# Kernel optimization log

Measured on AMD Instinct MI355X. Metric: run time of the kernel, lower is better.

The kernel has to match this reference:

```python
import jax, jax.numpy as jnp
import numpy as np

W, QN, H, HKV, D, HID = 2, 64, 28, 4, 128, 3584
FRAG_LENS = (8192, 4096, 2048)
THETA = 1e6


def rotate_half(x):
    x1, x2 = jnp.split(x, 2, axis=-1)
    return jnp.concatenate((-x2, x1), axis=-1)


def setup_inputs() -> dict:
    key = jax.random.key(0)
    ks = jax.random.split(key, 16)
    inp = {}
    inp['hidden_states'] = jax.random.normal(ks[0], (W, QN, HID), jnp.float32)
    inp['wq'] = 0.02 * jax.random.normal(ks[1], (H * D, HID), jnp.float32)
    inp['bq'] = 0.02 * jax.random.normal(ks[2], (H * D,), jnp.float32)
    inp['wo'] = 0.02 * jax.random.normal(ks[3], (HID, H * D), jnp.float32)
    for f, L in enumerate(FRAG_LENS):
        inp[f'keys{f}'] = jax.random.normal(ks[4 + f], (HKV, L, D), jnp.float32)
        inp[f'values{f}'] = jax.random.normal(ks[8 + f], (HKV, L, D), jnp.float32)
    # per-fragment query locations: frags 0,1 fully visible; frag 2 causal tail
    loc0 = jnp.full((W, QN), FRAG_LENS[0] - 1, jnp.int32)
    loc1 = jnp.full((W, QN), FRAG_LENS[1] - 1, jnp.int32)
    loc2 = jnp.broadcast_to(FRAG_LENS[2] - QN + jnp.arange(QN, dtype=jnp.int32), (W, QN))
    locations = jnp.stack([loc0, loc1, loc2], axis=0)  # [F, W, QN]
    inp['locations'] = locations
    # RoPE tables per fragment (HF half-rotation convention, base=1e6)
    inv_freq = 1.0 / (THETA ** (jnp.arange(0, D, 2, dtype=jnp.float32) / D))  # [D/2]
    ang = locations.astype(jnp.float32)[..., None] * inv_freq  # [F, W, QN, D/2]
    inp['cos'] = jnp.concatenate([jnp.cos(ang), jnp.cos(ang)], axis=-1)
    inp['sin'] = jnp.concatenate([jnp.sin(ang), jnp.sin(ang)], axis=-1)
    return inp


def _hogwild_attention(q, keys, values, cos, sin, locations, scale):
    # q: [W,H,QN,D]; keys[f]/values[f]: [HKV,L_f,D]; cos/sin: [F,W,QN,D]; locations: [F,W,QN]
    G = q.shape[1] // keys[0].shape[0]  # GQA group size
    logits = []
    for f in range(len(keys)):
        # fragment-specific RoPE on queries
        rq = q * cos[f][:, None] + rotate_half(q) * sin[f][:, None]  # [W,H,QN,D]
        kr = jnp.repeat(keys[f], G, axis=0)  # [H,L,D]
        att = jnp.einsum('whqd,hkd->whqk', rq.astype(jnp.float32), kr.astype(jnp.float32))
        kp = jnp.arange(keys[f].shape[1], dtype=jnp.int32)
        mask = kp[None, None, None, :] > locations[f][:, None, :, None]
        logits.append(jnp.where(mask, -jnp.inf, att))
    qk = jnp.concatenate(logits, axis=-1)  # [W,H,QN,Ktot]
    vals = jnp.concatenate([jnp.repeat(v, G, axis=0) for v in values], axis=1).astype(jnp.float32)
    p = jax.nn.softmax(scale * qk, axis=-1)
    return jnp.einsum('whqk,hkd->whqd', p, vals)  # [W,H,QN,D]


def reference(hidden_states, wq, bq, wo, keys0, keys1, keys2, values0, values1, values2, cos, sin, locations):
    scale = D ** -0.5
    q = hidden_states @ wq.T + bq  # [W,QN,H*D]
    q = q.reshape(W, QN, H, D).transpose(0, 2, 1, 3)  # [W,H,QN,D]
    out = _hogwild_attention(q, [keys0, keys1, keys2], [values0, values1, values2], cos, sin, locations, scale)
    out = out.astype(hidden_states.dtype).transpose(0, 2, 1, 3).reshape(W, QN, H * D)
    return out @ wo.T  # [W,QN,HID]
```

## Files before the change

### kernel.cpp

```cpp
#include <hip/hip_runtime.h>
#include <math.h>


typedef _Float16 f16;
typedef _Float16 h2 __attribute__((ext_vector_type(2)));
typedef _Float16 h4 __attribute__((ext_vector_type(4)));
typedef _Float16 h8 __attribute__((ext_vector_type(8)));
typedef float f32x16 __attribute__((ext_vector_type(16)));

static __device__ __forceinline__ float4 ld4(const float* p){ return *reinterpret_cast<const float4*>(p); }
static __device__ __forceinline__ void st4(float* p, const float4 v){ *reinterpret_cast<float4*>(p) = v; }
static __device__ __forceinline__ h2 pk(float a, float b){
  return __builtin_bit_cast(h2, __builtin_amdgcn_cvt_pkrtz(a, b));
}
static __device__ __forceinline__ h2 sw32(h2 v){
  int i = __builtin_bit_cast(int, v);
  i = __shfl_xor(i, 32, 64);
  return __builtin_bit_cast(h2, i);
}
static __device__ __forceinline__ h8 mk8(h2 a, h2 b, h2 c, h2 d){
  h8 r; r[0]=a[0]; r[1]=a[1]; r[2]=b[0]; r[3]=b[1]; r[4]=c[0]; r[5]=c[1]; r[6]=d[0]; r[7]=d[1]; return r;
}
static __device__ __forceinline__ h4 mk4(h2 a, h2 b){
  h4 r; r[0]=a[0]; r[1]=a[1]; r[2]=b[0]; r[3]=b[1]; return r;
}
static __device__ __forceinline__ h8 ld8h(const f16* p){
  const h4 a = *(const h4*)p;
  const h4 b = *(const h4*)(p + 4);
  h8 r; r[0]=a[0]; r[1]=a[1]; r[2]=a[2]; r[3]=a[3]; r[4]=b[0]; r[5]=b[1]; r[6]=b[2]; r[7]=b[3];
  return r;
}

#define SCALE 0.08838834764831845f

__global__ __launch_bounds__(256) void gemm_mfma_kernel(
    const float* __restrict__ A, const float* __restrict__ Bw,
    const float* __restrict__ bias, float* __restrict__ out, const int qlayout,
    float* __restrict__ Gpart, const int KS)
{
  __shared__ __align__(16) f16 Ah[128][68];
  __shared__ __align__(16) f16 Al[128][68];
  __shared__ __align__(16) f16 Bh[64][68];
  __shared__ __align__(16) f16 Bl[64][68];

  const int t = threadIdx.x;
  const int lane = t & 63;
  const int wv = t >> 6;
  const int l31 = lane & 31;
  const int hh = lane >> 5;
  const int nblk = blockIdx.x * 64;
  const int ks = blockIdx.y;
  const int kspan = 3584 / KS;
  const int kbeg = ks * kspan;

  f32x16 acc0, acc1;
#pragma unroll
  for (int g = 0; g < 16; ++g) { acc0[g] = 0.f; acc1[g] = 0.f; }

  for (int kc = kbeg; kc < kbeg + kspan; kc += 64) {
#pragma unroll
    for (int r = 0; r < 4; ++r) {
      const int li = r * 256 + t;
      const int m = li >> 3;
      const int k8 = (li & 7) * 8;
      const float* p = A + (size_t)m * 3584 + kc + k8;
      const float4 x0 = ld4(p), x1 = ld4(p + 4);
      const h2 a01 = pk(x0.x, x0.y), a23 = pk(x0.z, x0.w);
      const h2 a45 = pk(x1.x, x1.y), a67 = pk(x1.z, x1.w);
      const h2 r01 = pk(x0.x - (float)a01[0], x0.y - (float)a01[1]);
      const h2 r23 = pk(x0.z - (float)a23[0], x0.w - (float)a23[1]);
      const h2 r45 = pk(x1.x - (float)a45[0], x1.y - (float)a45[1]);
      const h2 r67 = pk(x1.z - (float)a67[0], x1.w - (float)a67[1]);
      *(h4*)&Ah[m][k8]     = mk4(a01, a23);
      *(h4*)&Ah[m][k8 + 4] = mk4(a45, a67);
      *(h4*)&Al[m][k8]     = mk4(r01, r23);
      *(h4*)&Al[m][k8 + 4] = mk4(r45, r67);
    }
#pragma unroll
    for (int r = 0; r < 2; ++r) {
      const int li = r * 256 + t;
      const int n = li >> 3;
      const int k8 = (li & 7) * 8;
      const float* p = Bw + (size_t)(nblk + n) * 3584 + kc + k8;
      const float4 x0 = ld4(p), x1 = ld4(p + 4);
      const h2 a01 = pk(x0.x, x0.y), a23 = pk(x0.z, x0.w);
      const h2 a45 = pk(x1.x, x1.y), a67 = pk(x1.z, x1.w);
      const h2 r01 = pk(x0.x - (float)a01[0], x0.y - (float)a01[1]);
      const h2 r23 = pk(x0.z - (float)a23[0], x0.w - (float)a23[1]);
      const h2 r45 = pk(x1.x - (float)a45[0], x1.y - (float)a45[1]);
      const h2 r67 = pk(x1.z - (float)a67[0], x1.w - (float)a67[1]);
      *(h4*)&Bh[n][k8]     = mk4(a01, a23);
      *(h4*)&Bh[n][k8 + 4] = mk4(a45, a67);
      *(h4*)&Bl[n][k8]     = mk4(r01, r23);
      *(h4*)&Bl[n][k8 + 4] = mk4(r45, r67);
    }
    __syncthreads();

#pragma unroll 2
    for (int k16 = 0; k16 < 4; ++k16) {
      const int ko = k16 * 16 + hh * 8;
      const h8 ah  = ld8h(&Ah[wv * 32 + l31][ko]);
      const h8 al  = ld8h(&Al[wv * 32 + l31][ko]);
      const h8 bh0 = ld8h(&Bh[l31][ko]);
      const h8 bl0 = ld8h(&Bl[l31][ko]);
      const h8 bh1 = ld8h(&Bh[32 + l31][ko]);
      const h8 bl1 = ld8h(&Bl[32 + l31][ko]);
      acc0 = __builtin_amdgcn_mfma_f32_32x32x16_f16(ah, bh0, acc0, 0, 0, 0);
      acc0 = __builtin_amdgcn_mfma_f32_32x32x16_f16(ah, bl0, acc0, 0, 0, 0);
      acc0 = __builtin_amdgcn_mfma_f32_32x32x16_f16(al, bh0, acc0, 0, 0, 0);
      acc1 = __builtin_amdgcn_mfma_f32_32x32x16_f16(ah, bh1, acc1, 0, 0, 0);
      acc1 = __builtin_amdgcn_mfma_f32_32x32x16_f16(ah, bl1, acc1, 0, 0, 0);
      acc1 = __builtin_amdgcn_mfma_f32_32x32x16_f16(al, bh1, acc1, 0, 0, 0);
    }
    __syncthreads();
  }

  if (Gpart) {
    float* gp = Gpart + (size_t)ks * 458752;
#pragma unroll
    for (int reg = 0; reg < 16; ++reg) {
      const int m = wv * 32 + (reg & 3) + 8 * (reg >> 2) + 4 * hh;
      gp[(size_t)m * 3584 + nblk + l31]      = acc0[reg];
      gp[(size_t)m * 3584 + nblk + 32 + l31] = acc1[reg];
    }
    return;
  }
#pragma unroll
  for (int reg = 0; reg < 16; ++reg) {
    const int m = wv * 32 + (reg & 3) + 8 * (reg >> 2) + 4 * hh;
#pragma unroll
    for (int nt = 0; nt < 2; ++nt) {
      const int n = nblk + nt * 32 + l31;
      float v = (nt ? acc1[reg] : acc0[reg]) + (bias ? bias[n] : 0.f);
      if (qlayout) {
        const int w = m >> 6, qn = m & 63, hcol = n >> 7, d = n & 127;
        out[(((size_t)(w * 28 + hcol)) * 64 + qn) * 128 + d] = v;
      } else {
        out[(size_t)m * 3584 + n] = v;
      }
    }
  }
}

__global__ __launch_bounds__(256) void gemm_reduce_kernel(
    const float* __restrict__ Gpart, const float* __restrict__ bias,
    float* __restrict__ out, const int KS, const int qlayout)
{
  const int idx = blockIdx.x * 256 + threadIdx.x;
  const int m = idx / 896;
  const int n = (idx - m * 896) * 4;
  float4 a = ld4(Gpart + (size_t)m * 3584 + n);
  for (int ss = 1; ss < KS; ++ss) {
    const float4 b = ld4(Gpart + (size_t)ss * 458752 + (size_t)m * 3584 + n);
    a.x += b.x; a.y += b.y; a.z += b.z; a.w += b.w;
  }
  if (bias) { a.x += bias[n]; a.y += bias[n + 1]; a.z += bias[n + 2]; a.w += bias[n + 3]; }
  if (qlayout) {
    const int w = m >> 6, qn = m & 63, hh = n >> 7, d = n & 127;
    st4(out + (((size_t)(w * 28 + hh)) * 64 + qn) * 128 + d, a);
  } else {
    st4(out + (size_t)m * 3584 + n, a);
  }
}

__global__ __launch_bounds__(256) void vtrans_kernel(
    const float* __restrict__ V0, const float* __restrict__ V1, const float* __restrict__ V2,
    f16* __restrict__ Vt)
{
  __shared__ __align__(16) f16 T[64 * 136];
  const int bid = blockIdx.x;
  const int kvh = bid / 224;
  const int g0 = (bid % 224) * 64;
  const int t = threadIdx.x;
#pragma unroll
  for (int rep = 0; rep < 8; ++rep) {
    const int li = rep * 256 + t;
    const int k = li >> 5;
    const int d0 = (li & 31) * 4;
    const int g = g0 + k;
    const float* src;
    if (g < 8192)       src = V0 + ((size_t)kvh * 8192 + g) * 128 + d0;
    else if (g < 12288) src = V1 + ((size_t)kvh * 4096 + (g - 8192)) * 128 + d0;
    else                src = V2 + ((size_t)kvh * 2048 + (g - 12288)) * 128 + d0;
    const float4 v = ld4(src);
    h2 x = pk(v.x, v.y), y = pk(v.z, v.w);
    h4 q4; q4[0] = x[0]; q4[1] = x[1]; q4[2] = y[0]; q4[3] = y[1];
    *(h4*)((char*)T + k * 272 + d0 * 2) = q4;
  }
  __syncthreads();
#pragma unroll
  for (int rep = 0; rep < 4; ++rep) {
    const int li = rep * 256 + t;
    const int d = li >> 3;
    const int kc = (li & 7) * 8;
    h8 o;
#pragma unroll
    for (int j = 0; j < 8; ++j) o[j] = T[(kc + j) * 136 + d];
    *(h8*)(Vt + ((size_t)kvh * 128 + d) * 14336 + g0 + kc) = o;
  }
}

__global__ __launch_bounds__(512, 4) void attn_mfma_kernel(
    const float* __restrict__ q_ws,
    const float* __restrict__ cosT, const float* __restrict__ sinT,
    const float* __restrict__ K0, const float* __restrict__ K1, const float* __restrict__ K2,
    const float* __restrict__ V0, const float* __restrict__ V1, const float* __restrict__ V2,
    const int* __restrict__ loc,
    const f16* __restrict__ Vt, const int vt16,
    float* __restrict__ attn,
    float* __restrict__ Opart, float* __restrict__ Ml, const int NS)
{
  union ShmU {
    struct { f16 k[128 * 128]; f16 vt[128 * 128]; } t;
    struct { float o[2][32 * 132]; float m[8][32]; float l[8][32];
             float lg[2][32]; float mg[2][32]; } e;
  };
  __shared__ __align__(16) ShmU S;
  __shared__ __align__(16) f16 RQ[64 * 128];

  int unit, s, h, w, kvh;
  if (NS > 1) {
    const int C = 4 * NS;
    const int combo = blockIdx.x % C;
    const int idx = blockIdx.x / C;
    kvh = combo / NS; s = combo % NS;
    const int hh7 = idx % 7;
    w = idx / 7;
    h = kvh * 7 + hh7;
    unit = w * 28 + h;
  } else {
    unit = blockIdx.x; s = 0;
    h = unit % 28; w = unit / 28; kvh = h / 7;
  }

  const int tiles_per = 112 / NS;
  const int tile0 = s * tiles_per;
  const int tile1 = tile0 + tiles_per;

  const int t = threadIdx.x;
  const int lane = t & 63;
  const int wv = t >> 6;
  const int g  = wv >> 2;
  const int wg = wv & 3;
  const int wk = wg * 32;
  const int l31 = lane & 31;
  const int hh = lane >> 5;

  const size_t qb = (size_t)unit * 64 * 128;

  const float* K0b = K0 + (size_t)kvh * 8192 * 128;
  const float* K1b = K1 + (size_t)kvh * 4096 * 128;
  const float* K2b = K2 + (size_t)kvh * 2048 * 128;
  const float* V0b = V0 + (size_t)kvh * 8192 * 128;
  const float* V1b = V1 + (size_t)kvh * 4096 * 128;
  const float* V2b = V2 + (size_t)kvh * 2048 * 128;
  const f16* Vtg = Vt ? (Vt + (size_t)kvh * 128 * 14336) : (const f16*)nullptr;

  f32x16 acc[4];
#pragma unroll
  for (int i = 0; i < 4; ++i)
#pragma unroll
    for (int gg = 0; gg < 16; ++gg) acc[i][gg] = 0.f;

  h8 rq[8];
  float m_run = -INFINITY, l_run = 0.f;
  int locq = 0;
  int fprev = -1;

  for (int tile = tile0; tile < tile1; ++tile) {
    int f, rel; const float *Kg, *Vg;
    if (tile < 64)      { f = 0; rel = tile * 128;        Kg = K0b; Vg = V0b; }
    else if (tile < 96) { f = 1; rel = (tile - 64) * 128; Kg = K1b; Vg = V1b; }
    else                { f = 2; rel = (tile - 96) * 128; Kg = K2b; Vg = V2b; }
    const int gcat = tile * 128;
    const bool fsw = (f != fprev);
    fprev = f;

    if (fsw) {
      const size_t cb = ((size_t)(f * 2 + w)) * 64 * 128;
#pragma unroll
      for (int rep = 0; rep < 2; ++rep) {
        const int qr = rep * 32 + (t >> 4);
        const int d0 = (t & 15) * 8;
        const float* qp = q_ws + qb + (size_t)qr * 128;
        const float4 a0 = ld4(qp + d0), a1 = ld4(qp + d0 + 4);
        const int pd = (d0 < 64) ? d0 + 64 : d0 - 64;
        const float4 r0 = ld4(qp + pd), r1 = ld4(qp + pd + 4);
        const float sg = (d0 < 64) ? -1.f : 1.f;
        const float* cp = cosT + cb + (size_t)qr * 128;
        const float* sp = sinT + cb + (size_t)qr * 128;
        const float4 c0 = ld4(cp + d0), c1 = ld4(cp + d0 + 4);
        const float4 s0 = ld4(sp + d0), s1 = ld4(sp + d0 + 4);
        h8 hv = mk8(pk(a0.x * c0.x + sg * r0.x * s0.x, a0.y * c0.y + sg * r0.y * s0.y),
                    pk(a0.z * c0.z + sg * r0.z * s0.z, a0.w * c0.w + sg * r0.w * s0.w),
                    pk(a1.x * c1.x + sg * r1.x * s1.x, a1.y * c1.y + sg * r1.y * s1.y),
                    pk(a1.z * c1.z + sg * r1.z * s1.z, a1.w * c1.w + sg * r1.w * s1.w));
        *(h8*)((char*)RQ + qr * 256 + ((d0 * 2) ^ ((qr & 7) << 4))) = hv;
      }
      locq = loc[(f * 2 + w) * 64 + g * 32 + l31];
    }

    if (vt16) {
#pragma unroll
      for (int rep = 0; rep < 4; ++rep) {
        const int r = rep * 32 + (t >> 4);
        const int c0 = (t & 15) * 8;
        const float* kp = Kg + (size_t)(rel + r) * 128 + c0;
        const float4 a = ld4(kp), b = ld4(kp + 4);
        const h8 v = mk8(pk(a.x, a.y), pk(a.z, a.w), pk(b.x, b.y), pk(b.z, b.w));
        *(h8*)((char*)S.t.k + r * 256 + ((c0 * 2) ^ ((r & 7) << 4))) = v;
      }
#pragma unroll
      for (int rep = 0; rep < 4; ++rep) {
        const int d = rep * 32 + (t >> 4);
        const int kc = (t & 15) * 8;
        const h8 v = *(const h8*)(Vtg + (size_t)d * 14336 + gcat + kc);
        *(h8*)((char*)S.t.vt + d * 256 + ((kc * 2) ^ ((d & 7) << 4))) = v;
      }
    } else {
#pragma unroll
      for (int rep = 0; rep < 8; ++rep) {
        const int r = rep * 16 + (t >> 5);
        const int d0 = (t & 31) * 4;
        const float4 v = ld4(Kg + (size_t)(rel + r) * 128 + d0);
        h2 x = pk(v.x, v.y), y = pk(v.z, v.w);
        h4 q4; q4[0] = x[0]; q4[1] = x[1]; q4[2] = y[0]; q4[3] = y[1];
        *(h4*)((char*)S.t.k + r * 256 + ((d0 * 2) ^ ((r & 7) << 4))) = q4;
      }
#pragma unroll
      for (int rep = 0; rep < 8; ++rep) {
        const int d = t & 127;
        const int k0 = (rep * 4 + (t >> 7)) * 4;
        const float* vp = Vg + (size_t)(rel + k0) * 128 + d;
        const float b0 = vp[0], b1 = vp[128], b2 = vp[256], b3 = vp[384];
        h2 x = pk(b0, b1), y = pk(b2, b3);
        h4 q4; q4[0] = x[0]; q4[1] = x[1]; q4[2] = y[0]; q4[3] = y[1];
        *(h4*)((char*)S.t.vt + d * 256 + ((k0 * 2) ^ ((d & 7) << 4))) = q4;
      }
    }
    __syncthreads();

    if (fsw) {
#pragma unroll
      for (int c = 0; c < 8; ++c)
        rq[c] = *(const h8*)((const char*)RQ + (g * 32 + l31) * 256 +
                             (((c * 32) + hh * 16) ^ ((l31 & 7) << 4)));
    }

    f32x16 sacc;
#pragma unroll
    for (int gg = 0; gg < 16; ++gg) sacc[gg] = 0.f;
    {
      const int r = wk + l31;
      const char* kb = (const char*)S.t.k + r * 256;
      const int sx = (r & 7) << 4;
      __builtin_amdgcn_s_setprio(1);
#pragma unroll
      for (int c = 0; c < 8; ++c) {
        const h8 a = *(const h8*)(kb + ((c * 32 + hh * 16) ^ sx));
        sacc = __builtin_amdgcn_mfma_f32_32x32x16_f16(a, rq[c], sacc, 0, 0, 0);
      }
      __builtin_amdgcn_s_setprio(0);
    }

    float p[16];
    float mt = -INFINITY;
#pragma unroll
    for (int gg = 0; gg < 16; ++gg) {
      const int kl = (gg & 3) + 8 * (gg >> 2) + 4 * hh;
      float z = sacc[gg] * SCALE;
      if (rel + wk + kl > locq) z = -INFINITY;
      p[gg] = z;
      mt = fmaxf(mt, z);
    }
    mt = fmaxf(mt, __shfl_xor(mt, 32, 64));
    if (!__all(mt <= m_run + 8.f)) {
      const float mn = fmaxf(m_run, mt);
      const float rr = __expf(m_run - mn);
      l_run *= rr;
#pragma unroll
      for (int i = 0; i < 4; ++i)
#pragma unroll
        for (int gg = 0; gg < 16; ++gg) acc[i][gg] *= rr;
      m_run = mn;
    }
    float ls = 0.f;
#pragma unroll
    for (int gg = 0; gg < 16; ++gg) { const float pe = __expf(p[gg] - m_run); p[gg] = pe; ls += pe; }
    l_run += ls + __shfl_xor(ls, 32, 64);

    h2 wvv[8], xvv[8];
#pragma unroll
    for (int gg = 0; gg < 8; ++gg) wvv[gg] = pk(p[2 * gg], p[2 * gg + 1]);
#pragma unroll
    for (int gg = 0; gg < 8; ++gg) xvv[gg] = sw32(wvv[gg]);
    const h8 bp0 = hh ? mk8(xvv[2], xvv[3], wvv[2], wvv[3]) : mk8(wvv[0], wvv[1], xvv[0], xvv[1]);
    const h8 bp1 = hh ? mk8(xvv[6], xvv[7], wvv[6], wvv[7]) : mk8(wvv[4], wvv[5], xvv[4], xvv[5]);

    {
      const char* vb = (const char*)S.t.vt;
      __builtin_amdgcn_s_setprio(1);
#pragma unroll
      for (int dt = 0; dt < 4; ++dt) {
        const int d = dt * 32 + l31;
        const int sx = (d & 7) << 4;
        const char* vrow = vb + d * 256;
        const h8 a0 = *(const h8*)(vrow + ((2 * (wk + hh * 8)) ^ sx));
        const h8 a1 = *(const h8*)(vrow + ((2 * (wk + 16 + hh * 8)) ^ sx));
        acc[dt] = __builtin_amdgcn_mfma_f32_32x32x16_f16(a0, bp0, acc[dt], 0, 0, 0);
        acc[dt] = __builtin_amdgcn_mfma_f32_32x32x16_f16(a1, bp1, acc[dt], 0, 0, 0);
      }
      __builtin_amdgcn_s_setprio(0);
    }
    __syncthreads();
  }

  if (lane < 32) { S.e.m[wv][l31] = m_run; S.e.l[wv][l31] = l_run; }
  {
    const float4 z4 = make_float4(0.f, 0.f, 0.f, 0.f);
    for (int i = t; i < 2 * 32 * 132 / 4; i += 512) ((float4*)S.e.o)[i] = z4;
  }
  __syncthreads();
  float M = -INFINITY;
#pragma unroll
  for (int j = 0; j < 4; ++j) M = fmaxf(M, S.e.m[g * 4 + j][l31]);
  float Lg = 0.f;
#pragma unroll
  for (int j = 0; j < 4; ++j) Lg += S.e.l[g * 4 + j][l31] * __expf(S.e.m[g * 4 + j][l31] - M);
  const float swf = __expf(m_run - M);
  if (wg == 0 && lane < 32) { S.e.lg[g][l31] = Lg; S.e.mg[g][l31] = M; }
  __syncthreads();

#pragma unroll
  for (int r = 0; r < 4; ++r) {
#pragma unroll
    for (int dt = 0; dt < 4; ++dt) {
#pragma unroll
      for (int gq = 0; gq < 4; ++gq) {
        if ((((dt * 2 + (gq >> 1)) - wg - r) & 3) == 0) {
          const int db = dt * 32 + 8 * gq + 4 * hh;
          float4* pp = (float4*)&S.e.o[g][l31 * 132 + db];
          float4 v = *pp;
          v.x += acc[dt][gq * 4 + 0] * swf;
          v.y += acc[dt][gq * 4 + 1] * swf;
          v.z += acc[dt][gq * 4 + 2] * swf;
          v.w += acc[dt][gq * 4 + 3] * swf;
          *pp = v;
        }
      }
    }
    __syncthreads();
  }

  {
    const int q = t >> 3;
    const int hf = q >> 5;
    const int qr = q & 31;
    const int d0 = (t & 7) * 16;
    const float* op = &S.e.o[hf][qr * 132 + d0];
    if (NS == 1) {
      const float invl = 1.f / S.e.lg[hf][qr];
      float* dst = attn + ((size_t)(w * 64 + q)) * 3584 + h * 128 + d0;
#pragma unroll
      for (int i = 0; i < 4; ++i)
        st4(dst + 4 * i, make_float4(op[4*i] * invl, op[4*i+1] * invl, op[4*i+2] * invl, op[4*i+3] * invl));
    } else {
      float* dst = Opart + (((size_t)unit * NS + s) * 64 + q) * 128 + d0;
#pragma unroll
      for (int i = 0; i < 4; ++i)
        st4(dst + 4 * i, make_float4(op[4*i], op[4*i+1], op[4*i+2], op[4*i+3]));
      if (t < 64) {
        float* mlp = Ml + ((size_t)unit * NS + s) * 128;
        mlp[t] = S.e.mg[t >> 5][t & 31];
        mlp[64 + t] = S.e.lg[t >> 5][t & 31];
      }
    }
  }
}

__global__ __launch_bounds__(512) void attn_combine_kernel(
    const float* __restrict__ Opart, const float* __restrict__ Ml,
    float* __restrict__ attn, const int NS)
{
  const int unit = blockIdx.x;
  const int h = unit % 28;
  const int w = unit / 28;
  const int t = threadIdx.x;
  const int q = t >> 3;
  const int d0 = (t & 7) * 16;

  float M = -INFINITY;
  for (int s = 0; s < NS; ++s) M = fmaxf(M, Ml[((size_t)unit * NS + s) * 128 + q]);
  float L = 0.f;
  float acc[16];
#pragma unroll
  for (int i = 0; i < 16; ++i) acc[i] = 0.f;
  for (int s = 0; s < NS; ++s) {
    const float ms = Ml[((size_t)unit * NS + s) * 128 + q];
    const float ls = Ml[((size_t)unit * NS + s) * 128 + 64 + q];
    const float wgt = __expf(ms - M);
    L += ls * wgt;
    const float* op = Opart + (((size_t)unit * NS + s) * 64 + q) * 128 + d0;
#pragma unroll
    for (int i = 0; i < 4; ++i) {
      const float4 v = ld4(op + 4 * i);
      acc[4 * i + 0] += v.x * wgt;
      acc[4 * i + 1] += v.y * wgt;
      acc[4 * i + 2] += v.z * wgt;
      acc[4 * i + 3] += v.w * wgt;
    }
  }
  const float invl = 1.f / L;
  float* dst = attn + ((size_t)(w * 64 + q)) * 3584 + h * 128 + d0;
#pragma unroll
  for (int i = 0; i < 4; ++i) {
    const float4 o = make_float4(acc[4 * i + 0] * invl, acc[4 * i + 1] * invl,
                                 acc[4 * i + 2] * invl, acc[4 * i + 3] * invl);
    st4(dst + 4 * i, o);
  }
}

extern "C" void kernel_launch(void* const* d_in, const int* in_sizes, int n_in,
                              void* d_out, int out_size, void* d_ws, size_t ws_size,
                              hipStream_t stream) {
  (void)n_in; (void)out_size;
  const float* hs = (const float*)d_in[0];
  const float* wq = (const float*)d_in[1];
  const float* bq = (const float*)d_in[2];
  const float* wo = (const float*)d_in[3];

  const float *K0, *V0, *K1, *V1, *K2, *V2, *cosT, *sinT;
  const int* loc;
  if (in_sizes[5] == in_sizes[4]) {
    K0 = (const float*)d_in[4]; V0 = (const float*)d_in[5];
    K1 = (const float*)d_in[6]; V1 = (const float*)d_in[7];
    K2 = (const float*)d_in[8]; V2 = (const float*)d_in[9];
    loc = (const int*)d_in[10];
    cosT = (const float*)d_in[11]; sinT = (const float*)d_in[12];
  } else {
    K0 = (const float*)d_in[4]; K1 = (const float*)d_in[5]; K2 = (const float*)d_in[6];
    V0 = (const float*)d_in[7]; V1 = (const float*)d_in[8]; V2 = (const float*)d_in[9];
    cosT = (const float*)d_in[10]; sinT = (const float*)d_in[11];
    loc = (const int*)d_in[12];
  }

  float* outp = (float*)d_out;
  float* attn = (float*)d_ws;
  char* base = (char*)d_ws;

  const size_t ATTN_B = (size_t)458752 * 4;
  const size_t RB = (size_t)4 * 128 * 14336 * 2;
  auto opartBytes = [](int ns){ return (size_t)56 * ns * 33280; };

  size_t off = ATTN_B;
  f16* Vt = nullptr; int vt16 = 0;
  float *Opart = nullptr, *Ml = nullptr, *Gpart = nullptr;
  int NS = 1, KS = 1;

  const bool haveR = (ws_size >= off + RB + opartBytes(2));
  if (haveR) {
    Vt = (f16*)(base + off); vt16 = 1;
    Gpart = (float*)(base + off); KS = 8;
    off += RB;
  }
  for (int cand = 8; cand >= 2; cand >>= 1) {
    if (ws_size >= off + opartBytes(cand)) {
      NS = cand;
      Opart = (float*)(base + off);
      Ml = Opart + (size_t)56 * cand * 64 * 128;
      off += opartBytes(cand);
      break;
    }
  }
  if (!haveR) {
    if (ws_size >= off + (size_t)8 * ATTN_B)      { KS = 8; Gpart = (float*)(base + off); }
    else if (ws_size >= off + (size_t)4 * ATTN_B) { KS = 4; Gpart = (float*)(base + off); }
  }

  if (KS > 1) {
    gemm_mfma_kernel<<<dim3(56, KS, 1), 256, 0, stream>>>(hs, wq, nullptr, nullptr, 1, Gpart, KS);
    gemm_reduce_kernel<<<448, 256, 0, stream>>>(Gpart, bq, outp, KS, 1);
  } else {
    gemm_mfma_kernel<<<dim3(56, 1, 1), 256, 0, stream>>>(hs, wq, bq, outp, 1, nullptr, 1);
  }

  if (vt16) vtrans_kernel<<<896, 256, 0, stream>>>(V0, V1, V2, Vt);

  const int grid = (NS > 1) ? 56 * NS : 56;
  attn_mfma_kernel<<<grid, 512, 0, stream>>>(
      outp, cosT, sinT, K0, K1, K2, V0, V1, V2, loc, Vt, vt16, attn, Opart, Ml, NS);
  if (NS > 1) attn_combine_kernel<<<56, 512, 0, stream>>>(Opart, Ml, attn, NS);

  if (KS > 1) {
    gemm_mfma_kernel<<<dim3(56, KS, 1), 256, 0, stream>>>(attn, wo, nullptr, nullptr, 0, Gpart, KS);
    gemm_reduce_kernel<<<448, 256, 0, stream>>>(Gpart, nullptr, outp, KS, 0);
  } else {
    gemm_mfma_kernel<<<dim3(56, 1, 1), 256, 0, stream>>>(attn, wo, nullptr, outp, 0, nullptr, 1);
  }
}
```

Measured before the change: 230.4 us.

## Load K and V MFMA operands directly from global memory, bypassing LDS staging

K and V tiles are no longer staged cooperatively through shared memory. Each wave now loads its MFMA operand fragments straight from global memory, converting fp32 K to fp16 in registers, and the per-tile __syncthreads barriers are removed. Shared memory shrinks to the rotated-Q buffer plus the epilogue scratch, which could raise occupancy. The trade-off is that K/V rows are re-read by the 8 waves per block instead of once, and the access patterns are less coalesced (especially the strided fp32 V fallback), so the kernel relies on L1/L2 absorbing that redundancy.

Result: slower. 530.6 us (+130.3%).

```diff
diff --git a/kernel.cpp b/kernel.cpp
--- a/kernel.cpp
+++ b/kernel.cpp
@@ -211,12 +211,11 @@
     float* __restrict__ Opart, float* __restrict__ Ml, const int NS)
 {
   union ShmU {
-    struct { f16 k[128 * 128]; f16 vt[128 * 128]; } t;
+    f16 rq[64 * 128];
     struct { float o[2][32 * 132]; float m[8][32]; float l[8][32];
              float lg[2][32]; float mg[2][32]; } e;
   };
   __shared__ __align__(16) ShmU S;
-  __shared__ __align__(16) f16 RQ[64 * 128];
 
   int unit, s, h, w, kvh;
   if (NS > 1) {
@@ -277,6 +276,7 @@
     fprev = f;
 
     if (fsw) {
+      __syncthreads();
       const size_t cb = ((size_t)(f * 2 + w)) * 64 * 128;
 #pragma unroll
       for (int rep = 0; rep < 2; ++rep) {
@@ -295,55 +295,13 @@
                     pk(a0.z * c0.z + sg * r0.z * s0.z, a0.w * c0.w + sg * r0.w * s0.w),
                     pk(a1.x * c1.x + sg * r1.x * s1.x, a1.y * c1.y + sg * r1.y * s1.y),
                     pk(a1.z * c1.z + sg * r1.z * s1.z, a1.w * c1.w + sg * r1.w * s1.w));
-        *(h8*)((char*)RQ + qr * 256 + ((d0 * 2) ^ ((qr & 7) << 4))) = hv;
+        *(h8*)((char*)S.rq + qr * 256 + ((d0 * 2) ^ ((qr & 7) << 4))) = hv;
       }
       locq = loc[(f * 2 + w) * 64 + g * 32 + l31];
-    }
-
-    if (vt16) {
-#pragma unroll
-      for (int rep = 0; rep < 4; ++rep) {
-        const int r = rep * 32 + (t >> 4);
-        const int c0 = (t & 15) * 8;
-        const float* kp = Kg + (size_t)(rel + r) * 128 + c0;
-        const float4 a = ld4(kp), b = ld4(kp + 4);
-        const h8 v = mk8(pk(a.x, a.y), pk(a.z, a.w), pk(b.x, b.y), pk(b.z, b.w));
-        *(h8*)((char*)S.t.k + r * 256 + ((c0 * 2) ^ ((r & 7) << 4))) = v;
-      }
-#pragma unroll
-      for (int rep = 0; rep < 4; ++rep) {
-        const int d = rep * 32 + (t >> 4);
-        const int kc = (t & 15) * 8;
-        const h8 v = *(const h8*)(Vtg + (size_t)d * 14336 + gcat + kc);
-        *(h8*)((char*)S.t.vt + d * 256 + ((kc * 2) ^ ((d & 7) << 4))) = v;
-      }
-    } else {
-#pragma unroll
-      for (int rep = 0; rep < 8; ++rep) {
-        const int r = rep * 16 + (t >> 5);
-        const int d0 = (t & 31) * 4;
-        const float4 v = ld4(Kg + (size_t)(rel + r) * 128 + d0);
-        h2 x = pk(v.x, v.y), y = pk(v.z, v.w);
-        h4 q4; q4[0] = x[0]; q4[1] = x[1]; q4[2] = y[0]; q4[3] = y[1];
-        *(h4*)((char*)S.t.k + r * 256 + ((d0 * 2) ^ ((r & 7) << 4))) = q4;
-      }
-#pragma unroll
-      for (int rep = 0; rep < 8; ++rep) {
-        const int d = t & 127;
-        const int k0 = (rep * 4 + (t >> 7)) * 4;
-        const float* vp = Vg + (size_t)(rel + k0) * 128 + d;
-        const float b0 = vp[0], b1 = vp[128], b2 = vp[256], b3 = vp[384];
-        h2 x = pk(b0, b1), y = pk(b2, b3);
-        h4 q4; q4[0] = x[0]; q4[1] = x[1]; q4[2] = y[0]; q4[3] = y[1];
-        *(h4*)((char*)S.t.vt + d * 256 + ((k0 * 2) ^ ((d & 7) << 4))) = q4;
-      }
-    }
-    __syncthreads();
-
-    if (fsw) {
+      __syncthreads();
 #pragma unroll
       for (int c = 0; c < 8; ++c)
-        rq[c] = *(const h8*)((const char*)RQ + (g * 32 + l31) * 256 +
+        rq[c] = *(const h8*)((const char*)S.rq + (g * 32 + l31) * 256 +
                              (((c * 32) + hh * 16) ^ ((l31 & 7) << 4)));
     }
 
@@ -351,13 +309,13 @@
 #pragma unroll
     for (int gg = 0; gg < 16; ++gg) sacc[gg] = 0.f;
     {
-      const int r = wk + l31;
-      const char* kb = (const char*)S.t.k + r * 256;
-      const int sx = (r & 7) << 4;
+      const float* kp = Kg + (size_t)(rel + wk + l31) * 128 + hh * 8;
       __builtin_amdgcn_s_setprio(1);
-#pragma unroll
+#pragma unroll 2
       for (int c = 0; c < 8; ++c) {
-        const h8 a = *(const h8*)(kb + ((c * 32 + hh * 16) ^ sx));
+        const float4 x0 = ld4(kp + c * 16);
+        const float4 x1 = ld4(kp + c * 16 + 4);
+        const h8 a = mk8(pk(x0.x, x0.y), pk(x0.z, x0.w), pk(x1.x, x1.y), pk(x1.z, x1.w));
         sacc = __builtin_amdgcn_mfma_f32_32x32x16_f16(a, rq[c], sacc, 0, 0, 0);
       }
       __builtin_amdgcn_s_setprio(0);
@@ -397,24 +355,38 @@
     const h8 bp0 = hh ? mk8(xvv[2], xvv[3], wvv[2], wvv[3]) : mk8(wvv[0], wvv[1], xvv[0], xvv[1]);
     const h8 bp1 = hh ? mk8(xvv[6], xvv[7], wvv[6], wvv[7]) : mk8(wvv[4], wvv[5], xvv[4], xvv[5]);
 
-    {
-      const char* vb = (const char*)S.t.vt;
-      __builtin_amdgcn_s_setprio(1);
+    __builtin_amdgcn_s_setprio(1);
+    if (vt16) {
+#pragma unroll 2
+      for (int dt = 0; dt < 4; ++dt) {
+        const f16* vp = Vtg + (size_t)(dt * 32 + l31) * 14336 + gcat + wk + hh * 8;
+        const h8 a0 = *(const h8*)vp;
+        const h8 a1 = *(const h8*)(vp + 16);
+        acc[dt] = __builtin_amdgcn_mfma_f32_32x32x16_f16(a0, bp0, acc[dt], 0, 0, 0);
+        acc[dt] = __builtin_amdgcn_mfma_f32_32x32x16_f16(a1, bp1, acc[dt], 0, 0, 0);
+      }
+    } else {
 #pragma unroll
       for (int dt = 0; dt < 4; ++dt) {
         const int d = dt * 32 + l31;
-        const int sx = (d & 7) << 4;
-        const char* vrow = vb + d * 256;
-        const h8 a0 = *(const h8*)(vrow + ((2 * (wk + hh * 8)) ^ sx));
-        const h8 a1 = *(const h8*)(vrow + ((2 * (wk + 16 + hh * 8)) ^ sx));
+        h8 a0, a1;
+#pragma unroll
+        for (int j = 0; j < 8; j += 2) {
+          const float v0 = Vg[(size_t)(rel + wk + hh * 8 + j) * 128 + d];
+          const float v1 = Vg[(size_t)(rel + wk + hh * 8 + j + 1) * 128 + d];
+          const h2 x = pk(v0, v1); a0[j] = x[0]; a0[j + 1] = x[1];
+          const float u0 = Vg[(size_t)(rel + wk + 16 + hh * 8 + j) * 128 + d];
+          const float u1 = Vg[(size_t)(rel + wk + 16 + hh * 8 + j + 1) * 128 + d];
+          const h2 y = pk(u0, u1); a1[j] = y[0]; a1[j + 1] = y[1];
+        }
         acc[dt] = __builtin_amdgcn_mfma_f32_32x32x16_f16(a0, bp0, acc[dt], 0, 0, 0);
         acc[dt] = __builtin_amdgcn_mfma_f32_32x32x16_f16(a1, bp1, acc[dt], 0, 0, 0);
       }
-      __builtin_amdgcn_s_setprio(0);
-    }
-    __syncthreads();
-  }
-
+    }
+    __builtin_amdgcn_s_setprio(0);
+  }
+
+  __syncthreads();
   if (lane < 32) { S.e.m[wv][l31] = m_run; S.e.l[wv][l31] = l_run; }
   {
     const float4 z4 = make_float4(0.f, 0.f, 0.f, 0.f);
```
